# Performance work log

Measured on AMD Instinct MI355X. Metric: run time of the kernel, lower is better.

Reference implementation:

```python
import jax, jax.numpy as jnp
import numpy as np

DAMP_MIN = jnp.asarray([0.001, 0.001], dtype=jnp.float32)
B = 4194304


def setup_inputs() -> dict:
    key = jax.random.key(0)
    ks = jax.random.split(key, 14)
    rn = lambda k, s: jax.random.normal(k, s, dtype=jnp.float32)
    return {
        "x": rn(ks[0], (B, 2)),
        "w_d1": rn(ks[1], (2, 16)),
        "w_d2": rn(ks[2], (16, 16)),
        "w_d3": rn(ks[3], (16, 2)),
        "w_o1": rn(ks[4], (2, 16)),
        "w_o2": rn(ks[5], (16, 16)),
        "w_o3": rn(ks[6], (16, 1)),
        "b_d1": rn(ks[7], (16,)),
        "b_d2": rn(ks[8], (16,)),
        "b_d3": rn(ks[9], (2,)),
        "b_o1": rn(ks[10], (16,)),
        "b_o2": rn(ks[11], (16,)),
        "b_o3": rn(ks[12], (1,)),
    }


def reference(x, w_d1, w_d2, w_d3, w_o1, w_o2, w_o3,
              b_d1, b_d2, b_d3, b_o1, b_o2, b_o3) -> jnp.ndarray:
    # diag branch: 3-layer tanh MLP -> relu -> +damp_min -> * x   [B, 2]
    d = jnp.tanh(x @ w_d1 + b_d1)
    d = jnp.tanh(d @ w_d2 + b_d2)
    d3 = d @ w_d3 + b_d3
    d3r = (jax.nn.relu(d3) + DAMP_MIN) * x  # diag elements of L

    # off-diag branch: 3-layer tanh MLP -> scalar per sample   [B, 1]
    o = jnp.tanh(x @ w_o1 + b_o1)
    o = jnp.tanh(o @ w_o2 + b_o2)
    o3 = o @ w_o3 + b_o3

    # L = [[a, 0], [c, b]];  D_i = (L L^T) x_i, closed form for 2x2:
    # L L^T = [[a^2, a*c], [a*c, c^2 + b^2]]
    a = d3r[:, 0]
    b = d3r[:, 1]
    c = o3[:, 0]
    x0 = x[:, 0]
    x1 = x[:, 1]
    D0 = a * a * x0 + a * c * x1
    D1 = a * c * x0 + (c * c + b * b) * x1
    return jnp.stack([D0, D1], axis=1)  # [B, 2]
```

## Files before the change

kernel.cpp:

```cpp
#include <hip/hip_runtime.h>

#define BTOT 4194304
#define MPW 4

typedef __attribute__((ext_vector_type(4))) float f32x4;
typedef __attribute__((ext_vector_type(8))) short bf16x8;

#define KLOG 2.88539008177792681472f

__device__ __forceinline__ short f2bf(float f) {
  union { float f; unsigned u; } v; v.f = f;
  unsigned u = v.u;
  unsigned r = (u + 0x7FFFu + ((u >> 16) & 1u)) >> 16;
  return (short)r;
}
__device__ __forceinline__ float bf2f(short s) {
  union { unsigned u; float f; } v; v.u = ((unsigned)(unsigned short)s) << 16;
  return v.f;
}
__device__ __forceinline__ float tanh_pre(float y) {
  float t = __builtin_amdgcn_exp2f(y);
  float r = __builtin_amdgcn_rcpf(1.0f + t);
  return __builtin_fmaf(-2.0f, r, 1.0f);
}

__device__ __forceinline__ void pack_hilo(const float* h, bf16x8& bh, bf16x8& bl) {
  union U { unsigned w[4]; bf16x8 v; } H, L;
  #pragma unroll
  for (int jw = 0; jw < 4; ++jw) {
    float h0 = h[2 * jw], h1 = h[2 * jw + 1];
    unsigned u0 = __builtin_bit_cast(unsigned, h0);
    unsigned u1 = __builtin_bit_cast(unsigned, h1);
    float hi0 = __builtin_bit_cast(float, u0 & 0xFFFF0000u);
    float hi1 = __builtin_bit_cast(float, u1 & 0xFFFF0000u);
    float lo0 = h0 - hi0;
    float lo1 = h1 - hi1;
    unsigned v0 = __builtin_bit_cast(unsigned, lo0);
    unsigned v1 = __builtin_bit_cast(unsigned, lo1);
    H.w[jw] = __builtin_amdgcn_perm(u1, u0, 0x07060302u);
    L.w[jw] = __builtin_amdgcn_perm(v1, v0, 0x07060302u);
  }
  bh = H.v; bl = L.v;
}

__global__ __launch_bounds__(256, 4)
void damping_kernel(const float* __restrict__ x,
                    const float* __restrict__ w_d1, const float* __restrict__ w_d2,
                    const float* __restrict__ w_d3, const float* __restrict__ w_o1,
                    const float* __restrict__ w_o2, const float* __restrict__ w_o3,
                    const float* __restrict__ b_d1, const float* __restrict__ b_d2,
                    const float* __restrict__ b_d3, const float* __restrict__ b_o1,
                    const float* __restrict__ b_o2, const float* __restrict__ b_o3,
                    float* __restrict__ out)
{
  const int tid  = blockIdx.x * blockDim.x + threadIdx.x;
  const int wave = tid >> 6;
  const int l    = threadIdx.x & 63;
  const int g    = l >> 4;
  const int c16  = l & 15;
  const int kbase = g * 8;

  float W0[8], W1[8], B1[8];
  #pragma unroll
  for (int j = 0; j < 8; ++j) {
    int f = kbase + j;
    if (f < 16) { W0[j] = KLOG * w_d1[f];      W1[j] = KLOG * w_d1[16 + f];      B1[j] = KLOG * b_d1[f]; }
    else        { W0[j] = KLOG * w_o1[f - 16]; W1[j] = KLOG * w_o1[16 + f - 16]; B1[j] = KLOG * b_o1[f - 16]; }
  }
  bf16x8 Adh, Adl, Aoh, Aol;
  #pragma unroll
  for (int j = 0; j < 8; ++j) {
    int k = kbase + j;
    float ad = (k < 16)  ? KLOG * w_d2[k * 16 + c16]        : 0.0f;
    float ao = (k >= 16) ? KLOG * w_o2[(k - 16) * 16 + c16] : 0.0f;
    short adh = f2bf(ad); Adh[j] = adh; Adl[j] = f2bf(ad - bf2f(adh));
    short aoh = f2bf(ao); Aoh[j] = aoh; Aol[j] = f2bf(ao - bf2f(aoh));
  }
  f32x4 Cd0, Co0;
  float Wd30[4], Wd31[4], Wo3[4];
  #pragma unroll
  for (int i = 0; i < 4; ++i) {
    int f = g * 4 + i;
    Cd0[i] = KLOG * b_d2[f]; Co0[i] = KLOG * b_o2[f];
    Wd30[i] = w_d3[f * 2]; Wd31[i] = w_d3[f * 2 + 1]; Wo3[i] = w_o3[f];
  }
  const float bq0 = b_d3[0] * 0.25f, bq1 = b_d3[1] * 0.25f, bqo = b_o3[0] * 0.25f;

  for (int m = 0; m < MPW; ++m) {
    const int mbase = (wave * MPW + m) * 64;

    float2 xv4[4];
    #pragma unroll
    for (int t = 0; t < 4; ++t)
      xv4[t] = ((const float2*)x)[mbase + t * 16 + c16];

    float o0 = 0.f, o1 = 0.f;
    #pragma unroll
    for (int t = 0; t < 4; ++t) {
      const float2 xv = xv4[t];

      float h[8];
      #pragma unroll
      for (int j = 0; j < 8; ++j)
        h[j] = tanh_pre(__builtin_fmaf(xv.y, W1[j], __builtin_fmaf(xv.x, W0[j], B1[j])));

      bf16x8 bh, bl;
      pack_hilo(h, bh, bl);

      f32x4 accd = Cd0, acco = Co0;
      accd = __builtin_amdgcn_mfma_f32_16x16x32_bf16(Adh, bh, accd, 0, 0, 0);
      acco = __builtin_amdgcn_mfma_f32_16x16x32_bf16(Aoh, bh, acco, 0, 0, 0);
      accd = __builtin_amdgcn_mfma_f32_16x16x32_bf16(Adh, bl, accd, 0, 0, 0);
      acco = __builtin_amdgcn_mfma_f32_16x16x32_bf16(Aoh, bl, acco, 0, 0, 0);
      accd = __builtin_amdgcn_mfma_f32_16x16x32_bf16(Adl, bh, accd, 0, 0, 0);
      acco = __builtin_amdgcn_mfma_f32_16x16x32_bf16(Aol, bh, acco, 0, 0, 0);

      float pd0 = bq0, pd1 = bq1, po = bqo;
      #pragma unroll
      for (int i = 0; i < 4; ++i) {
        float dt = tanh_pre(accd[i]);
        float ot = tanh_pre(acco[i]);
        pd0 = __builtin_fmaf(dt, Wd30[i], pd0);
        pd1 = __builtin_fmaf(dt, Wd31[i], pd1);
        po  = __builtin_fmaf(ot, Wo3[i],  po);
      }
      pd0 += __shfl_xor(pd0, 16); pd0 += __shfl_xor(pd0, 32);
      pd1 += __shfl_xor(pd1, 16); pd1 += __shfl_xor(pd1, 32);
      po  += __shfl_xor(po, 16);  po  += __shfl_xor(po, 32);

      float a = (fmaxf(pd0, 0.f) + 0.001f) * xv.x;
      float b = (fmaxf(pd1, 0.f) + 0.001f) * xv.y;
      float c = po;
      float D0 = a * __builtin_fmaf(a, xv.x, c * xv.y);
      float s  = __builtin_fmaf(c, c, b * b);
      float D1 = __builtin_fmaf(a * c, xv.x, s * xv.y);

      if (t == g) { o0 = D0; o1 = D1; }
    }
    ((float2*)out)[mbase + l] = make_float2(o0, o1);
  }
}

extern "C" void kernel_launch(void* const* d_in, const int* in_sizes, int n_in,
                              void* d_out, int out_size, void* d_ws, size_t ws_size,
                              hipStream_t stream) {
  const float* x    = (const float*)d_in[0];
  const float* w_d1 = (const float*)d_in[1];
  const float* w_d2 = (const float*)d_in[2];
  const float* w_d3 = (const float*)d_in[3];
  const float* w_o1 = (const float*)d_in[4];
  const float* w_o2 = (const float*)d_in[5];
  const float* w_o3 = (const float*)d_in[6];
  const float* b_d1 = (const float*)d_in[7];
  const float* b_d2 = (const float*)d_in[8];
  const float* b_d3 = (const float*)d_in[9];
  const float* b_o1 = (const float*)d_in[10];
  const float* b_o2 = (const float*)d_in[11];
  const float* b_o3 = (const float*)d_in[12];
  float* out = (float*)d_out;

  const int waves  = BTOT / (64 * MPW);
  const int blocks = waves / 4;
  damping_kernel<<<blocks, 256, 0, stream>>>(x, w_d1, w_d2, w_d3, w_o1, w_o2, w_o3,
                                             b_d1, b_d2, b_d3, b_o1, b_o2, b_o3, out);
}
```

Before: 174.4 us.

## Batch tanh reciprocals and move layer-3 reduction onto MFMA instead of shuffles

Replaces the per-element reciprocal in tanh with a batched scheme that computes one rcp per four values from running products, and clamps inputs so those products cannot overflow. Layer-3 (the 16→2 and 16→1 projections) becomes a split-bf16 hi/lo MFMA that accumulates over the four sample tiles, replacing the per-tile cross-lane shuffle reductions and the masked select. The final epilogue reloads x per lane and runs once per 64 samples instead of four times. The trade is extra multiplies, three more MFMAs per tile, extra packing work and more registers for the A3 fragments, plus a small accuracy change from the product-based reciprocal and the clamp.

```diff
diff --git a/kernel.cpp b/kernel.cpp
--- a/kernel.cpp
+++ b/kernel.cpp
@@ -7,6 +7,7 @@
 typedef __attribute__((ext_vector_type(8))) short bf16x8;
 
 #define KLOG 2.88539008177792681472f
+#define YCLAMP 30.0f
 
 __device__ __forceinline__ short f2bf(float f) {
   union { float f; unsigned u; } v; v.f = f;
@@ -18,10 +19,26 @@
   union { unsigned u; float f; } v; v.u = ((unsigned)(unsigned short)s) << 16;
   return v.f;
 }
-__device__ __forceinline__ float tanh_pre(float y) {
-  float t = __builtin_amdgcn_exp2f(y);
-  float r = __builtin_amdgcn_rcpf(1.0f + t);
-  return __builtin_fmaf(-2.0f, r, 1.0f);
+
+__device__ __forceinline__ void tanh_b4(const float* y, float* o) {
+  float u0 = 1.0f + __builtin_amdgcn_exp2f(y[0]);
+  float u1 = 1.0f + __builtin_amdgcn_exp2f(y[1]);
+  float u2 = 1.0f + __builtin_amdgcn_exp2f(y[2]);
+  float u3 = 1.0f + __builtin_amdgcn_exp2f(y[3]);
+  float p01  = u0 * u1;
+  float p012 = p01 * u2;
+  float P    = p012 * u3;
+  float r  = __builtin_amdgcn_rcpf(P);
+  float i3 = r * p012;
+  float r3 = r * u3;
+  float i2 = r3 * p01;
+  float r2 = r3 * u2;
+  float i1 = r2 * u0;
+  float i0 = r2 * u1;
+  o[0] = __builtin_fmaf(-2.0f, i0, 1.0f);
+  o[1] = __builtin_fmaf(-2.0f, i1, 1.0f);
+  o[2] = __builtin_fmaf(-2.0f, i2, 1.0f);
+  o[3] = __builtin_fmaf(-2.0f, i3, 1.0f);
 }
 
 __device__ __forceinline__ void pack_hilo(const float* h, bf16x8& bh, bf16x8& bl) {
@@ -77,14 +94,30 @@
     short aoh = f2bf(ao); Aoh[j] = aoh; Aol[j] = f2bf(ao - bf2f(aoh));
   }
   f32x4 Cd0, Co0;
-  float Wd30[4], Wd31[4], Wo3[4];
   #pragma unroll
   for (int i = 0; i < 4; ++i) {
     int f = g * 4 + i;
     Cd0[i] = KLOG * b_d2[f]; Co0[i] = KLOG * b_o2[f];
-    Wd30[i] = w_d3[f * 2]; Wd31[i] = w_d3[f * 2 + 1]; Wo3[i] = w_o3[f];
-  }
-  const float bq0 = b_d3[0] * 0.25f, bq1 = b_d3[1] * 0.25f, bqo = b_o3[0] * 0.25f;
+  }
+
+  const int rr = c16 & 3, tt = c16 >> 2;
+  bf16x8 A3h[4], A3l[4];
+  #pragma unroll
+  for (int t = 0; t < 4; ++t) {
+    #pragma unroll
+    for (int j = 0; j < 8; ++j) {
+      float val = 0.0f;
+      if (t == tt) {
+        if (rr == 0 && j < 4)  val = w_d3[(4 * g + j) * 2 + 0];
+        if (rr == 1 && j < 4)  val = w_d3[(4 * g + j) * 2 + 1];
+        if (rr == 2 && j >= 4) val = w_o3[4 * g + j - 4];
+      }
+      short vh = f2bf(val);
+      A3h[t][j] = vh;
+      A3l[t][j] = f2bf(val - bf2f(vh));
+    }
+  }
+  const float b30 = b_d3[0], b31 = b_d3[1], b3o = b_o3[0];
 
   for (int m = 0; m < MPW; ++m) {
     const int mbase = (wave * MPW + m) * 64;
@@ -94,15 +127,20 @@
     for (int t = 0; t < 4; ++t)
       xv4[t] = ((const float2*)x)[mbase + t * 16 + c16];
 
-    float o0 = 0.f, o1 = 0.f;
+    f32x4 acc3;
+    acc3[0] = b30; acc3[1] = b31; acc3[2] = b3o; acc3[3] = 0.0f;
+
     #pragma unroll
     for (int t = 0; t < 4; ++t) {
       const float2 xv = xv4[t];
 
-      float h[8];
+      float y[8];
       #pragma unroll
       for (int j = 0; j < 8; ++j)
-        h[j] = tanh_pre(__builtin_fmaf(xv.y, W1[j], __builtin_fmaf(xv.x, W0[j], B1[j])));
+        y[j] = fminf(__builtin_fmaf(xv.y, W1[j], __builtin_fmaf(xv.x, W0[j], B1[j])), YCLAMP);
+      float h[8];
+      tanh_b4(y, h);
+      tanh_b4(y + 4, h + 4);
 
       bf16x8 bh, bl;
       pack_hilo(h, bh, bl);
@@ -115,29 +153,32 @@
       accd = __builtin_amdgcn_mfma_f32_16x16x32_bf16(Adl, bh, accd, 0, 0, 0);
       acco = __builtin_amdgcn_mfma_f32_16x16x32_bf16(Aol, bh, acco, 0, 0, 0);
 
-      float pd0 = bq0, pd1 = bq1, po = bqo;
+      float y2[8];
       #pragma unroll
       for (int i = 0; i < 4; ++i) {
-        float dt = tanh_pre(accd[i]);
-        float ot = tanh_pre(acco[i]);
-        pd0 = __builtin_fmaf(dt, Wd30[i], pd0);
-        pd1 = __builtin_fmaf(dt, Wd31[i], pd1);
-        po  = __builtin_fmaf(ot, Wo3[i],  po);
+        y2[i]     = fminf(accd[i], YCLAMP);
+        y2[4 + i] = fminf(acco[i], YCLAMP);
       }
-      pd0 += __shfl_xor(pd0, 16); pd0 += __shfl_xor(pd0, 32);
-      pd1 += __shfl_xor(pd1, 16); pd1 += __shfl_xor(pd1, 32);
-      po  += __shfl_xor(po, 16);  po  += __shfl_xor(po, 32);
-
-      float a = (fmaxf(pd0, 0.f) + 0.001f) * xv.x;
-      float b = (fmaxf(pd1, 0.f) + 0.001f) * xv.y;
-      float c = po;
-      float D0 = a * __builtin_fmaf(a, xv.x, c * xv.y);
-      float s  = __builtin_fmaf(c, c, b * b);
-      float D1 = __builtin_fmaf(a * c, xv.x, s * xv.y);
-
-      if (t == g) { o0 = D0; o1 = D1; }
+      float h2[8];
+      tanh_b4(y2, h2);
+      tanh_b4(y2 + 4, h2 + 4);
+
+      bf16x8 b3h, b3l;
+      pack_hilo(h2, b3h, b3l);
+
+      acc3 = __builtin_amdgcn_mfma_f32_16x16x32_bf16(A3h[t], b3h, acc3, 0, 0, 0);
+      acc3 = __builtin_amdgcn_mfma_f32_16x16x32_bf16(A3h[t], b3l, acc3, 0, 0, 0);
+      acc3 = __builtin_amdgcn_mfma_f32_16x16x32_bf16(A3l[t], b3h, acc3, 0, 0, 0);
     }
-    ((float2*)out)[mbase + l] = make_float2(o0, o1);
+
+    const float2 xs = ((const float2*)x)[mbase + l];
+    float a = (fmaxf(acc3[0], 0.0f) + 0.001f) * xs.x;
+    float b = (fmaxf(acc3[1], 0.0f) + 0.001f) * xs.y;
+    float c = acc3[2];
+    float D0 = a * __builtin_fmaf(a, xs.x, c * xs.y);
+    float s  = __builtin_fmaf(c, c, b * b);
+    float D1 = __builtin_fmaf(a * c, xs.x, s * xs.y);
+    ((float2*)out)[mbase + l] = make_float2(D0, D1);
   }
 }
 
```

After: 194.5 us. +11.5%, slower.

## Move third layer onto MFMA and cut hi/lo split to single bf16 activations

Applied to the files above, without the earlier changes.

Replaces the manual hi/lo bf16 split of the activations with a single hardware v_cvt_pk_bf16_f32 pack. This cuts layer-2 MFMAs from six to four per tile, since the activations are no longer split and only the weights keep a hi/lo pair. The third layer, which was per-lane FMAs followed by cross-lane shuffle reductions, becomes one accumulating MFMA per tile against a sparse weight matrix that places each tile's outputs directly in the owning lane. This removes the shuffles and the redundant epilogue over four tiles. In exchange, activations and the third-layer weights lose precision through single bf16 rounding, and x is reloaded once for the epilogue.

```diff
diff --git a/kernel.cpp b/kernel.cpp
--- a/kernel.cpp
+++ b/kernel.cpp
@@ -18,29 +18,23 @@
   union { unsigned u; float f; } v; v.u = ((unsigned)(unsigned short)s) << 16;
   return v.f;
 }
+
 __device__ __forceinline__ float tanh_pre(float y) {
   float t = __builtin_amdgcn_exp2f(y);
   float r = __builtin_amdgcn_rcpf(1.0f + t);
   return __builtin_fmaf(-2.0f, r, 1.0f);
 }
 
-__device__ __forceinline__ void pack_hilo(const float* h, bf16x8& bh, bf16x8& bl) {
-  union U { unsigned w[4]; bf16x8 v; } H, L;
+__device__ __forceinline__ unsigned cvt_pk(float lo, float hi) {
+  unsigned r;
+  asm("v_cvt_pk_bf16_f32 %0, %1, %2" : "=v"(r) : "v"(lo), "v"(hi));
+  return r;
+}
+__device__ __forceinline__ bf16x8 pack8(const float* h) {
+  union { unsigned w[4]; bf16x8 v; } U;
   #pragma unroll
-  for (int jw = 0; jw < 4; ++jw) {
-    float h0 = h[2 * jw], h1 = h[2 * jw + 1];
-    unsigned u0 = __builtin_bit_cast(unsigned, h0);
-    unsigned u1 = __builtin_bit_cast(unsigned, h1);
-    float hi0 = __builtin_bit_cast(float, u0 & 0xFFFF0000u);
-    float hi1 = __builtin_bit_cast(float, u1 & 0xFFFF0000u);
-    float lo0 = h0 - hi0;
-    float lo1 = h1 - hi1;
-    unsigned v0 = __builtin_bit_cast(unsigned, lo0);
-    unsigned v1 = __builtin_bit_cast(unsigned, lo1);
-    H.w[jw] = __builtin_amdgcn_perm(u1, u0, 0x07060302u);
-    L.w[jw] = __builtin_amdgcn_perm(v1, v0, 0x07060302u);
-  }
-  bh = H.v; bl = L.v;
+  for (int jw = 0; jw < 4; ++jw) U.w[jw] = cvt_pk(h[2 * jw], h[2 * jw + 1]);
+  return U.v;
 }
 
 __global__ __launch_bounds__(256, 4)
@@ -77,14 +71,30 @@
     short aoh = f2bf(ao); Aoh[j] = aoh; Aol[j] = f2bf(ao - bf2f(aoh));
   }
   f32x4 Cd0, Co0;
-  float Wd30[4], Wd31[4], Wo3[4];
   #pragma unroll
   for (int i = 0; i < 4; ++i) {
     int f = g * 4 + i;
     Cd0[i] = KLOG * b_d2[f]; Co0[i] = KLOG * b_o2[f];
-    Wd30[i] = w_d3[f * 2]; Wd31[i] = w_d3[f * 2 + 1]; Wo3[i] = w_o3[f];
   }
-  const float bq0 = b_d3[0] * 0.25f, bq1 = b_d3[1] * 0.25f, bqo = b_o3[0] * 0.25f;
+
+  const int rr = c16 & 3, tt = c16 >> 2;
+  bf16x8 A3h[4];
+  #pragma unroll
+  for (int t = 0; t < 4; ++t) {
+    #pragma unroll
+    for (int j = 0; j < 8; ++j) {
+      float val = 0.0f;
+      if (t == tt) {
+        if (rr == 0 && j < 4)  val = w_d3[(4 * g + j) * 2 + 0];
+        if (rr == 1 && j < 4)  val = w_d3[(4 * g + j) * 2 + 1];
+        if (rr == 2 && j >= 4) val = w_o3[4 * g + j - 4];
+      }
+      A3h[t][j] = f2bf(val);
+    }
+  }
+  const float b30 = b_d3[0], b31 = b_d3[1], b3o = b_o3[0];
+
+  const float2* x2 = (const float2*)x;
 
   for (int m = 0; m < MPW; ++m) {
     const int mbase = (wave * MPW + m) * 64;
@@ -92,9 +102,11 @@
     float2 xv4[4];
     #pragma unroll
     for (int t = 0; t < 4; ++t)
-      xv4[t] = ((const float2*)x)[mbase + t * 16 + c16];
+      xv4[t] = x2[mbase + t * 16 + c16];
 
-    float o0 = 0.f, o1 = 0.f;
+    f32x4 acc3;
+    acc3[0] = b30; acc3[1] = b31; acc3[2] = b3o; acc3[3] = 0.0f;
+
     #pragma unroll
     for (int t = 0; t < 4; ++t) {
       const float2 xv = xv4[t];
@@ -104,40 +116,33 @@
       for (int j = 0; j < 8; ++j)
         h[j] = tanh_pre(__builtin_fmaf(xv.y, W1[j], __builtin_fmaf(xv.x, W0[j], B1[j])));
 
-      bf16x8 bh, bl;
-      pack_hilo(h, bh, bl);
+      bf16x8 b1f = pack8(h);
 
       f32x4 accd = Cd0, acco = Co0;
-      accd = __builtin_amdgcn_mfma_f32_16x16x32_bf16(Adh, bh, accd, 0, 0, 0);
-      acco = __builtin_amdgcn_mfma_f32_16x16x32_bf16(Aoh, bh, acco, 0, 0, 0);
-      accd = __builtin_amdgcn_mfma_f32_16x16x32_bf16(Adh, bl, accd, 0, 0, 0);
-      acco = __builtin_amdgcn_mfma_f32_16x16x32_bf16(Aoh, bl, acco, 0, 0, 0);
-      accd = __builtin_amdgcn_mfma_f32_16x16x32_bf16(Adl, bh, accd, 0, 0, 0);
-      acco = __builtin_amdgcn_mfma_f32_16x16x32_bf16(Aol, bh, acco, 0, 0, 0);
+      accd = __builtin_amdgcn_mfma_f32_16x16x32_bf16(Adh, b1f, accd, 0, 0, 0);
+      accd = __builtin_amdgcn_mfma_f32_16x16x32_bf16(Adl, b1f, accd, 0, 0, 0);
+      acco = __builtin_amdgcn_mfma_f32_16x16x32_bf16(Aoh, b1f, acco, 0, 0, 0);
+      acco = __builtin_amdgcn_mfma_f32_16x16x32_bf16(Aol, b1f, acco, 0, 0, 0);
 
-      float pd0 = bq0, pd1 = bq1, po = bqo;
+      float h2[8];
       #pragma unroll
       for (int i = 0; i < 4; ++i) {
-        float dt = tanh_pre(accd[i]);
-        float ot = tanh_pre(acco[i]);
-        pd0 = __builtin_fmaf(dt, Wd30[i], pd0);
-        pd1 = __builtin_fmaf(dt, Wd31[i], pd1);
-        po  = __builtin_fmaf(ot, Wo3[i],  po);
+        h2[i]     = tanh_pre(accd[i]);
+        h2[4 + i] = tanh_pre(acco[i]);
       }
-      pd0 += __shfl_xor(pd0, 16); pd0 += __shfl_xor(pd0, 32);
-      pd1 += __shfl_xor(pd1, 16); pd1 += __shfl_xor(pd1, 32);
-      po  += __shfl_xor(po, 16);  po  += __shfl_xor(po, 32);
+      bf16x8 b3f = pack8(h2);
 
-      float a = (fmaxf(pd0, 0.f) + 0.001f) * xv.x;
-      float b = (fmaxf(pd1, 0.f) + 0.001f) * xv.y;
-      float c = po;
-      float D0 = a * __builtin_fmaf(a, xv.x, c * xv.y);
-      float s  = __builtin_fmaf(c, c, b * b);
-      float D1 = __builtin_fmaf(a * c, xv.x, s * xv.y);
+      acc3 = __builtin_amdgcn_mfma_f32_16x16x32_bf16(A3h[t], b3f, acc3, 0, 0, 0);
+    }
 
-      if (t == g) { o0 = D0; o1 = D1; }
-    }
-    ((float2*)out)[mbase + l] = make_float2(o0, o1);
+    const float2 xs = x2[mbase + l];
+    float a = (fmaxf(acc3[0], 0.0f) + 0.001f) * xs.x;
+    float b = (fmaxf(acc3[1], 0.0f) + 0.001f) * xs.y;
+    float c = acc3[2];
+    float D0 = a * __builtin_fmaf(a, xs.x, c * xs.y);
+    float s  = __builtin_fmaf(c, c, b * b);
+    float D1 = __builtin_fmaf(a * c, xs.x, s * xs.y);
+    ((float2*)out)[mbase + l] = make_float2(D0, D1);
   }
 }
 
```

Result: faster. 165.2 us (-5.3%).
